# Optimization experiments

Measured on AMD Instinct MI355X. Metric: run time of the kernel, lower is better.

The kernel has to match this reference:

```python
import jax, jax.numpy as jnp
import numpy as np

B, T, C = 2, 2048, 2048
NH, NKV, D = 16, 4, 128
N_REP = NH // NKV
THETA = 10000.0


def setup_inputs() -> dict:
    key = jax.random.key(0)
    ks = jax.random.split(key, 5)
    s = 0.02
    return {
        "x": jax.random.normal(ks[0], (B, T, C), dtype=jnp.float32),
        "Wq": jax.random.normal(ks[1], (C, C), dtype=jnp.float32) * s,
        "Wk": jax.random.normal(ks[2], (NKV * D, C), dtype=jnp.float32) * s,
        "Wv": jax.random.normal(ks[3], (NKV * D, C), dtype=jnp.float32) * s,
        "Wo": jax.random.normal(ks[4], (C, C), dtype=jnp.float32) * s,
    }


def _rope(t):
    # t: (B, H, T, D); rotate pairs (even, odd) by angle pos * theta_i
    inv_freq = 1.0 / (THETA ** (jnp.arange(0, D, 2, dtype=jnp.float32) / D))  # (D/2,)
    ang = jnp.arange(T, dtype=jnp.float32)[:, None] * inv_freq[None, :]       # (T, D/2)
    cos, sin = jnp.cos(ang), jnp.sin(ang)
    te, to = t[..., 0::2], t[..., 1::2]
    re = te * cos - to * sin
    ro = te * sin + to * cos
    return jnp.stack([re, ro], axis=-1).reshape(t.shape).astype(t.dtype)


def reference(x, Wq, Wk, Wv, Wo):
    # Projections (Linear: y = x @ W.T)
    q = (x @ Wq.T).reshape(B, T, NH, D).transpose(0, 2, 1, 3)    # (B,NH,T,D)
    k = (x @ Wk.T).reshape(B, T, NKV, D).transpose(0, 2, 1, 3)   # (B,NKV,T,D)
    v = (x @ Wv.T).reshape(B, T, NKV, D).transpose(0, 2, 1, 3)
    q = _rope(q)
    k = _rope(k)
    # GQA: group query heads per kv head instead of materializing repeated K/V
    qg = q.reshape(B, NKV, N_REP, T, D)                          # (B,G,R,T,D)
    scale = 1.0 / jnp.sqrt(jnp.float32(D))
    scores = jnp.einsum("bgrtd,bgsd->bgrts", qg, k) * scale      # (B,G,R,T,T)
    causal = jnp.tril(jnp.ones((T, T), dtype=bool))
    scores = jnp.where(causal, scores, jnp.finfo(scores.dtype).min)
    attn = jax.nn.softmax(scores, axis=-1)
    out = jnp.einsum("bgrts,bgsd->bgrtd", attn, v)               # (B,G,R,T,D)
    out = out.reshape(B, NH, T, D).transpose(0, 2, 1, 3).reshape(B, T, C)
    return out @ Wo.T
```

## Files before the change

kernel.cpp:

```cpp
#include <hip/hip_runtime.h>
#include <hip/hip_bf16.h>
#include <stdint.h>

#define B_   2
#define T_   2048
#define C_   2048
#define NH_  16
#define NKV_ 4
#define D_   128
#define NREP_ 4

typedef __attribute__((ext_vector_type(8))) short bf16x8;
typedef __attribute__((ext_vector_type(4))) float f32x4;

__device__ inline short f2bs(float f) {
    __hip_bfloat16 h = __float2bfloat16(f);
    return *reinterpret_cast<short*>(&h);
}
__device__ inline float bs2f(unsigned short s) {
    __hip_bfloat16 h = *reinterpret_cast<__hip_bfloat16*>(&s);
    return __bfloat162float(h);
}

__device__ inline void gl_lds16(const __hip_bfloat16* g, __hip_bfloat16* l) {
    __builtin_amdgcn_global_load_lds(
        (const __attribute__((address_space(1))) unsigned int*)g,
        (__attribute__((address_space(3))) unsigned int*)l,
        16, 0, 0);
}

__global__ void cvt_f32_bf16(const float* __restrict__ src,
                             __hip_bfloat16* __restrict__ dst, int n) {
    int i = (blockIdx.x * blockDim.x + threadIdx.x) * 4;
    if (i >= n) return;
    float4 v = *reinterpret_cast<const float4*>(src + i);
    short4 o;
    o.x = f2bs(v.x); o.y = f2bs(v.y); o.z = f2bs(v.z); o.w = f2bs(v.w);
    *reinterpret_cast<short4*>(dst + i) = o;
}

__device__ inline void storeC(float* p, float v) { *p = v; }
__device__ inline void storeC(__hip_bfloat16* p, float v) { *p = __float2bfloat16(v); }

template <typename OutT>
__global__ __launch_bounds__(256) void gemm_bt(const __hip_bfloat16* __restrict__ A,
                                               const __hip_bfloat16* __restrict__ Bm,
                                               OutT* __restrict__ Cm,
                                               int M, int N, int K) {
    __shared__ __hip_bfloat16 As[128 * 32];
    __shared__ __hip_bfloat16 Bs[128 * 32];
    const int tid  = threadIdx.x;
    const int lane = tid & 63;
    const int wv   = tid >> 6;
    const int m0 = blockIdx.y * 128, n0 = blockIdx.x * 128;
    const int wm = (wv >> 1) * 64, wn = (wv & 1) * 64;
    const int q16 = lane >> 4, r16 = lane & 15;

    f32x4 acc[4][4] = {};

    const int lrow = tid >> 2;
    const int lcol = (tid & 3) * 8;
    const __hip_bfloat16* aG = A  + (size_t)(m0 + lrow) * K + lcol;
    const __hip_bfloat16* bG = Bm + (size_t)(n0 + lrow) * K + lcol;
    __hip_bfloat16* aL = As + tid * 8;
    __hip_bfloat16* bL = Bs + tid * 8;

    for (int k0 = 0; k0 < K; k0 += 32) {
        __syncthreads();
        gl_lds16(aG + k0,          aL);
        gl_lds16(aG + 64 * K + k0, aL + 2048);
        gl_lds16(bG + k0,          bL);
        gl_lds16(bG + 64 * K + k0, bL + 2048);
        __syncthreads();
        bf16x8 af[4], bfr[4];
#pragma unroll
        for (int i = 0; i < 4; i++)
            af[i] = *reinterpret_cast<const bf16x8*>(As + (wm + i * 16 + r16) * 32 + q16 * 8);
#pragma unroll
        for (int j = 0; j < 4; j++)
            bfr[j] = *reinterpret_cast<const bf16x8*>(Bs + (wn + j * 16 + r16) * 32 + q16 * 8);
#pragma unroll
        for (int i = 0; i < 4; i++)
#pragma unroll
            for (int j = 0; j < 4; j++)
                acc[i][j] = __builtin_amdgcn_mfma_f32_16x16x32_bf16(af[i], bfr[j], acc[i][j], 0, 0, 0);
    }

#pragma unroll
    for (int i = 0; i < 4; i++)
#pragma unroll
        for (int j = 0; j < 4; j++)
#pragma unroll
            for (int r = 0; r < 4; r++) {
                int row = m0 + wm + i * 16 + q16 * 4 + r;
                int col = n0 + wn + j * 16 + r16;
                storeC(&Cm[(size_t)row * N + col], acc[i][j][r]);
            }
}

__global__ void rope_scatter(const __hip_bfloat16* __restrict__ y,
                             __hip_bfloat16* __restrict__ qo,
                             __hip_bfloat16* __restrict__ ko,
                             __hip_bfloat16* __restrict__ vT) {
    int idx = blockIdx.x * blockDim.x + threadIdx.x;
    if (idx >= (B_ * T_) * 1536) return;
    int m = idx / 1536, pc = idx % 1536;
    int b = m / T_, t = m % T_;
    int n = pc * 2;
    ushort2 uv = *reinterpret_cast<const ushort2*>(y + (size_t)m * 3072 + n);
    float e = bs2f(uv.x), od = bs2f(uv.y);

    if (n < 2560) {
        int nn = (n < 2048) ? n : (n - 2048);
        int dloc = nn & 127;
        int p = dloc >> 1;
        float inv = __expf(-(float)p * (9.210340371976184f / 64.0f));
        float ang = (float)t * inv;
        float c = cosf(ang), s = sinf(ang);
        float re = e * c - od * s;
        float ro = e * s + od * c;
        ushort2 w;
        w.x = (unsigned short)f2bs(re);
        w.y = (unsigned short)f2bs(ro);
        if (n < 2048) {
            int h = n >> 7;
            *reinterpret_cast<ushort2*>(qo + ((size_t)(b * NH_ + h) * T_ + t) * D_ + dloc) = w;
        } else {
            int h = nn >> 7;
            *reinterpret_cast<ushort2*>(ko + ((size_t)(b * NKV_ + h) * T_ + t) * D_ + dloc) = w;
        }
    } else {
        int nn = n - 2560;
        int h = nn >> 7, d = nn & 127;
        __hip_bfloat16* base = vT + (size_t)(b * NKV_ + h) * D_ * T_;
        base[(size_t)d * T_ + t]       = __float2bfloat16(e);
        base[(size_t)(d + 1) * T_ + t] = __float2bfloat16(od);
    }
}

__global__ __launch_bounds__(256, 3) void attn_kernel(const __hip_bfloat16* __restrict__ Q,
                                                      const __hip_bfloat16* __restrict__ Kt,
                                                      const __hip_bfloat16* __restrict__ Vt,
                                                      __hip_bfloat16* __restrict__ Ao) {
    __shared__ __hip_bfloat16 Ks[2][4096];
    __shared__ __hip_bfloat16 Vs[2][4096];
    __shared__ __hip_bfloat16 Pl[4][1280];

    const int lane = threadIdx.x & 63, wv = threadIdx.x >> 6;
    const int bg = blockIdx.y;
    const int tb = (int)(gridDim.x - 1) - (int)blockIdx.x;
    const int b = bg >> 2, g = bg & 3;
    const int h = g * 4 + wv;
    const int t0 = tb * 32;
    const int q16 = lane >> 4, r16 = lane & 15;

    const __hip_bfloat16* qh = Q + ((size_t)((b * NH_ + h) * T_) + t0) * D_;
    const __hip_bfloat16* kh = Kt + (size_t)(b * NKV_ + g) * T_ * D_;
    const __hip_bfloat16* vh = Vt + (size_t)(b * NKV_ + g) * D_ * T_;

    bf16x8 bqA[4], bqB[4];
#pragma unroll
    for (int kk = 0; kk < 4; kk++) {
        bqA[kk] = *reinterpret_cast<const bf16x8*>(qh + (size_t)r16 * D_ + kk * 32 + q16 * 8);
        bqB[kk] = *reinterpret_cast<const bf16x8*>(qh + (size_t)(16 + r16) * D_ + kk * 32 + q16 * 8);
    }

    float liA = 0.f, liB = 0.f;
    f32x4 oA[8], oB[8];
#pragma unroll
    for (int d = 0; d < 8; d++) {
        oA[d] = (f32x4){0.f, 0.f, 0.f, 0.f};
        oB[d] = (f32x4){0.f, 0.f, 0.f, 0.f};
    }

    const float SCL2 = 0.088388347648318447f * 1.4426950408889634f;
    const int tqA = t0 + r16;
    const int tqB = t0 + 16 + r16;
    const int nIter = tb + 1;

    const __hip_bfloat16* gK = kh + (size_t)((wv & 1) * 16 + r16) * D_ + q16 * 8;
    const __hip_bfloat16* gV = vh + (size_t)(((wv - 2) * 4) * 16 + r16) * T_ + q16 * 8;

#define STAGE(bufi, s0_)                                                        \
    do {                                                                        \
        if (wv < 2) {                                                           \
            const __hip_bfloat16* gp = gK + (size_t)(s0_) * D_;                 \
            __hip_bfloat16* lp = &Ks[bufi][(wv * 4) * 512] + lane * 8;          \
            gl_lds16(gp,      lp);                                              \
            gl_lds16(gp + 32, lp + 512);                                        \
            gl_lds16(gp + 64, lp + 1024);                                       \
            gl_lds16(gp + 96, lp + 1536);                                       \
        } else {                                                                \
            const __hip_bfloat16* gp = gV + (s0_);                              \
            __hip_bfloat16* lp = &Vs[bufi][((wv - 2) * 4) * 512] + lane * 8;    \
            gl_lds16(gp,                      lp);                              \
            gl_lds16(gp + (size_t)16 * T_,    lp + 512);                        \
            gl_lds16(gp + (size_t)32 * T_,    lp + 1024);                       \
            gl_lds16(gp + (size_t)48 * T_,    lp + 1536);                       \
        }                                                                       \
    } while (0)

    STAGE(0, 0);

    for (int it = 0; it < nIter; it++) {
        const int s0 = it * 32;
        const int cur = it & 1;
        __syncthreads();
        if (it + 1 < nIter) STAGE(cur ^ 1, s0 + 32);

        f32x4 sc0A = (f32x4){0.f, 0.f, 0.f, 0.f};
        f32x4 sc1A = (f32x4){0.f, 0.f, 0.f, 0.f};
        f32x4 sc0B = (f32x4){0.f, 0.f, 0.f, 0.f};
        f32x4 sc1B = (f32x4){0.f, 0.f, 0.f, 0.f};
        {
            bf16x8 ak[4];
#pragma unroll
            for (int kk = 0; kk < 4; kk++)
                ak[kk] = *reinterpret_cast<const bf16x8*>(&Ks[cur][kk * 512] + lane * 8);
#pragma unroll
            for (int kk = 0; kk < 4; kk++) {
                sc0A = __builtin_amdgcn_mfma_f32_16x16x32_bf16(ak[kk], bqA[kk], sc0A, 0, 0, 0);
                sc0B = __builtin_amdgcn_mfma_f32_16x16x32_bf16(ak[kk], bqB[kk], sc0B, 0, 0, 0);
            }
#pragma unroll
            for (int kk = 0; kk < 4; kk++)
                ak[kk] = *reinterpret_cast<const bf16x8*>(&Ks[cur][(4 + kk) * 512] + lane * 8);
#pragma unroll
            for (int kk = 0; kk < 4; kk++) {
                sc1A = __builtin_amdgcn_mfma_f32_16x16x32_bf16(ak[kk], bqA[kk], sc1A, 0, 0, 0);
                sc1B = __builtin_amdgcn_mfma_f32_16x16x32_bf16(ak[kk], bqB[kk], sc1B, 0, 0, 0);
            }
        }

        ushort4 w0A, w1A, w0B, w1B;
        float psA = 0.f, psB = 0.f;
#pragma unroll
        for (int r = 0; r < 4; r++) {
            int s_a = s0 + q16 * 4 + r;
            float pa0 = (s_a <= tqA)      ? __builtin_amdgcn_exp2f(sc0A[r] * SCL2) : 0.f;
            float pa1 = (s_a + 16 <= tqA) ? __builtin_amdgcn_exp2f(sc1A[r] * SCL2) : 0.f;
            float pb0 = (s_a <= tqB)      ? __builtin_amdgcn_exp2f(sc0B[r] * SCL2) : 0.f;
            float pb1 = (s_a + 16 <= tqB) ? __builtin_amdgcn_exp2f(sc1B[r] * SCL2) : 0.f;
            psA += pa0 + pa1;
            psB += pb0 + pb1;
            ((unsigned short*)&w0A)[r] = (unsigned short)f2bs(pa0);
            ((unsigned short*)&w1A)[r] = (unsigned short)f2bs(pa1);
            ((unsigned short*)&w0B)[r] = (unsigned short)f2bs(pb0);
            ((unsigned short*)&w1B)[r] = (unsigned short)f2bs(pb1);
        }
        liA += psA;
        liB += psB;

        *reinterpret_cast<ushort4*>(&Pl[wv][r16 * 40 + q16 * 4]) = w0A;
        *reinterpret_cast<ushort4*>(&Pl[wv][r16 * 40 + 16 + q16 * 4]) = w1A;
        *reinterpret_cast<ushort4*>(&Pl[wv][640 + r16 * 40 + q16 * 4]) = w0B;
        *reinterpret_cast<ushort4*>(&Pl[wv][640 + r16 * 40 + 16 + q16 * 4]) = w1B;
        asm volatile("s_waitcnt lgkmcnt(0)" ::: "memory");
        bf16x8 pfA = *reinterpret_cast<const bf16x8*>(&Pl[wv][r16 * 40 + q16 * 8]);
        bf16x8 pfB = *reinterpret_cast<const bf16x8*>(&Pl[wv][640 + r16 * 40 + q16 * 8]);

#pragma unroll
        for (int d = 0; d < 8; d++) {
            bf16x8 bv = *reinterpret_cast<const bf16x8*>(&Vs[cur][d * 512] + lane * 8);
            oA[d] = __builtin_amdgcn_mfma_f32_16x16x32_bf16(pfA, bv, oA[d], 0, 0, 0);
            oB[d] = __builtin_amdgcn_mfma_f32_16x16x32_bf16(pfB, bv, oB[d], 0, 0, 0);
        }
    }

    liA += __shfl_xor(liA, 16);
    liA += __shfl_xor(liA, 32);
    liB += __shfl_xor(liB, 16);
    liB += __shfl_xor(liB, 32);
#pragma unroll
    for (int r = 0; r < 4; r++) {
        float lrA = __shfl(liA, q16 * 4 + r, 16);
        float lrB = __shfl(liB, q16 * 4 + r, 16);
        float invA = 1.0f / lrA;
        float invB = 1.0f / lrB;
        int tA = t0 + q16 * 4 + r;
        __hip_bfloat16* dstA = Ao + (size_t)(b * T_ + tA) * C_ + h * D_ + r16;
        __hip_bfloat16* dstB = dstA + (size_t)16 * C_;
#pragma unroll
        for (int d = 0; d < 8; d++) {
            dstA[d * 16] = __float2bfloat16(oA[d][r] * invA);
            dstB[d * 16] = __float2bfloat16(oB[d][r] * invB);
        }
    }
#undef STAGE
}

extern "C" void kernel_launch(void* const* d_in, const int* in_sizes, int n_in,
                              void* d_out, int out_size, void* d_ws, size_t ws_size,
                              hipStream_t stream) {
    const float* x  = (const float*)d_in[0];
    const float* Wq = (const float*)d_in[1];
    const float* Wk = (const float*)d_in[2];
    const float* Wv = (const float*)d_in[3];
    const float* Wo = (const float*)d_in[4];
    float* out = (float*)d_out;
    char* ws = (char*)d_ws;

    __hip_bfloat16* xb   = (__hip_bfloat16*)(ws + 0);
    __hip_bfloat16* wcat = (__hip_bfloat16*)(ws + 16777216);
    __hip_bfloat16* wob  = (__hip_bfloat16*)(ws + 29360128);
    __hip_bfloat16* yq   = (__hip_bfloat16*)(ws + 37748736);
    __hip_bfloat16* qatt = (__hip_bfloat16*)(ws + 62914560);
    __hip_bfloat16* katt = (__hip_bfloat16*)(ws + 79691776);
    __hip_bfloat16* vT   = (__hip_bfloat16*)(ws + 83886080);
    __hip_bfloat16* aout = (__hip_bfloat16*)(ws + 88080384);

    const int thr = 256;
    cvt_f32_bf16<<<(B_ * T_ * C_ / 4 + thr - 1) / thr, thr, 0, stream>>>(x, xb, B_ * T_ * C_);
    cvt_f32_bf16<<<(C_ * C_ / 4 + thr - 1) / thr, thr, 0, stream>>>(Wq, wcat, C_ * C_);
    cvt_f32_bf16<<<(512 * 2048 / 4 + thr - 1) / thr, thr, 0, stream>>>(Wk, wcat + C_ * C_, 512 * 2048);
    cvt_f32_bf16<<<(512 * 2048 / 4 + thr - 1) / thr, thr, 0, stream>>>(Wv, wcat + C_ * C_ + 512 * 2048, 512 * 2048);
    cvt_f32_bf16<<<(C_ * C_ / 4 + thr - 1) / thr, thr, 0, stream>>>(Wo, wob, C_ * C_);

    gemm_bt<__hip_bfloat16><<<dim3(24, 32), 256, 0, stream>>>(xb, wcat, yq, 4096, 3072, 2048);

    rope_scatter<<<(B_ * T_ * 1536 + thr - 1) / thr, thr, 0, stream>>>(yq, qatt, katt, vT);

    attn_kernel<<<dim3(64, 8), 256, 0, stream>>>(qatt, katt, vT, aout);

    gemm_bt<float><<<dim3(16, 32), 256, 0, stream>>>(aout, wob, out, 4096, 2048, 2048);
}
```

Before: 351.4 us.

## Split long causal attention rows into two KV halves with combine pass

Query tiles in the second half of the sequence are now handled by two blocks, each covering half of the KV range. Each writes unnormalized fp32 partial outputs and row sums to workspace, and a new combine kernel adds the halves and normalizes. This evens out the per-block work of causal attention and raises the block count from 512 to 768. Fully unmasked tiles also skip the causal compare. The split relies on the kernel having no running-max subtraction, so partial results add directly. The cost is extra fp32 traffic, one extra launch, and reuse of workspace regions (xb, yq) that are already dead at that point.

```diff
diff --git a/kernel.cpp b/kernel.cpp
--- a/kernel.cpp
+++ b/kernel.cpp
@@ -141,14 +141,23 @@
 __global__ __launch_bounds__(256, 3) void attn_kernel(const __hip_bfloat16* __restrict__ Q,
                                                       const __hip_bfloat16* __restrict__ Kt,
                                                       const __hip_bfloat16* __restrict__ Vt,
-                                                      __hip_bfloat16* __restrict__ Ao) {
+                                                      __hip_bfloat16* __restrict__ Ao,
+                                                      float* __restrict__ O0,
+                                                      float* __restrict__ O1,
+                                                      float* __restrict__ l0p,
+                                                      float* __restrict__ l1p) {
     __shared__ __hip_bfloat16 Ks[2][4096];
     __shared__ __hip_bfloat16 Vs[2][4096];
     __shared__ __hip_bfloat16 Pl[4][1280];
 
     const int lane = threadIdx.x & 63, wv = threadIdx.x >> 6;
     const int bg = blockIdx.y;
-    const int tb = (int)(gridDim.x - 1) - (int)blockIdx.x;
+    const int u  = (int)blockIdx.x;
+    int tb, nIt, sIdx;
+    if (u < 32)      { tb = u;      nIt = tb + 1;      sIdx = -1; }
+    else if (u < 64) { tb = u;      nIt = 32;          sIdx = 0;  }
+    else             { tb = u - 32; nIt = tb + 1 - 32; sIdx = 1;  }
+    const int sBase = (sIdx == 1) ? 1024 : 0;
     const int b = bg >> 2, g = bg & 3;
     const int h = g * 4 + wv;
     const int t0 = tb * 32;
@@ -176,7 +185,6 @@
     const float SCL2 = 0.088388347648318447f * 1.4426950408889634f;
     const int tqA = t0 + r16;
     const int tqB = t0 + 16 + r16;
-    const int nIter = tb + 1;
 
     const __hip_bfloat16* gK = kh + (size_t)((wv & 1) * 16 + r16) * D_ + q16 * 8;
     const __hip_bfloat16* gV = vh + (size_t)(((wv - 2) * 4) * 16 + r16) * T_ + q16 * 8;
@@ -200,13 +208,13 @@
         }                                                                       \
     } while (0)
 
-    STAGE(0, 0);
-
-    for (int it = 0; it < nIter; it++) {
-        const int s0 = it * 32;
-        const int cur = it & 1;
+    STAGE(0, sBase);
+
+    for (int j = 0; j < nIt; j++) {
+        const int s0 = sBase + j * 32;
+        const int cur = j & 1;
         __syncthreads();
-        if (it + 1 < nIter) STAGE(cur ^ 1, s0 + 32);
+        if (j + 1 < nIt) STAGE(cur ^ 1, s0 + 32);
 
         f32x4 sc0A = (f32x4){0.f, 0.f, 0.f, 0.f};
         f32x4 sc1A = (f32x4){0.f, 0.f, 0.f, 0.f};
@@ -234,19 +242,35 @@
 
         ushort4 w0A, w1A, w0B, w1B;
         float psA = 0.f, psB = 0.f;
-#pragma unroll
-        for (int r = 0; r < 4; r++) {
-            int s_a = s0 + q16 * 4 + r;
-            float pa0 = (s_a <= tqA)      ? __builtin_amdgcn_exp2f(sc0A[r] * SCL2) : 0.f;
-            float pa1 = (s_a + 16 <= tqA) ? __builtin_amdgcn_exp2f(sc1A[r] * SCL2) : 0.f;
-            float pb0 = (s_a <= tqB)      ? __builtin_amdgcn_exp2f(sc0B[r] * SCL2) : 0.f;
-            float pb1 = (s_a + 16 <= tqB) ? __builtin_amdgcn_exp2f(sc1B[r] * SCL2) : 0.f;
-            psA += pa0 + pa1;
-            psB += pb0 + pb1;
-            ((unsigned short*)&w0A)[r] = (unsigned short)f2bs(pa0);
-            ((unsigned short*)&w1A)[r] = (unsigned short)f2bs(pa1);
-            ((unsigned short*)&w0B)[r] = (unsigned short)f2bs(pb0);
-            ((unsigned short*)&w1B)[r] = (unsigned short)f2bs(pb1);
+        if (s0 + 32 > t0) {
+#pragma unroll
+            for (int r = 0; r < 4; r++) {
+                int s_a = s0 + q16 * 4 + r;
+                float pa0 = (s_a <= tqA)      ? __builtin_amdgcn_exp2f(sc0A[r] * SCL2) : 0.f;
+                float pa1 = (s_a + 16 <= tqA) ? __builtin_amdgcn_exp2f(sc1A[r] * SCL2) : 0.f;
+                float pb0 = (s_a <= tqB)      ? __builtin_amdgcn_exp2f(sc0B[r] * SCL2) : 0.f;
+                float pb1 = (s_a + 16 <= tqB) ? __builtin_amdgcn_exp2f(sc1B[r] * SCL2) : 0.f;
+                psA += pa0 + pa1;
+                psB += pb0 + pb1;
+                ((unsigned short*)&w0A)[r] = (unsigned short)f2bs(pa0);
+                ((unsigned short*)&w1A)[r] = (unsigned short)f2bs(pa1);
+                ((unsigned short*)&w0B)[r] = (unsigned short)f2bs(pb0);
+                ((unsigned short*)&w1B)[r] = (unsigned short)f2bs(pb1);
+            }
+        } else {
+#pragma unroll
+            for (int r = 0; r < 4; r++) {
+                float pa0 = __builtin_amdgcn_exp2f(sc0A[r] * SCL2);
+                float pa1 = __builtin_amdgcn_exp2f(sc1A[r] * SCL2);
+                float pb0 = __builtin_amdgcn_exp2f(sc0B[r] * SCL2);
+                float pb1 = __builtin_amdgcn_exp2f(sc1B[r] * SCL2);
+                psA += pa0 + pa1;
+                psB += pb0 + pb1;
+                ((unsigned short*)&w0A)[r] = (unsigned short)f2bs(pa0);
+                ((unsigned short*)&w1A)[r] = (unsigned short)f2bs(pa1);
+                ((unsigned short*)&w0B)[r] = (unsigned short)f2bs(pb0);
+                ((unsigned short*)&w1B)[r] = (unsigned short)f2bs(pb1);
+            }
         }
         liA += psA;
         liB += psB;
@@ -271,22 +295,62 @@
     liA += __shfl_xor(liA, 32);
     liB += __shfl_xor(liB, 16);
     liB += __shfl_xor(liB, 32);
-#pragma unroll
-    for (int r = 0; r < 4; r++) {
-        float lrA = __shfl(liA, q16 * 4 + r, 16);
-        float lrB = __shfl(liB, q16 * 4 + r, 16);
-        float invA = 1.0f / lrA;
-        float invB = 1.0f / lrB;
-        int tA = t0 + q16 * 4 + r;
-        __hip_bfloat16* dstA = Ao + (size_t)(b * T_ + tA) * C_ + h * D_ + r16;
-        __hip_bfloat16* dstB = dstA + (size_t)16 * C_;
-#pragma unroll
-        for (int d = 0; d < 8; d++) {
-            dstA[d * 16] = __float2bfloat16(oA[d][r] * invA);
-            dstB[d * 16] = __float2bfloat16(oB[d][r] * invB);
+
+    if (sIdx < 0) {
+#pragma unroll
+        for (int r = 0; r < 4; r++) {
+            float lrA = __shfl(liA, q16 * 4 + r, 16);
+            float lrB = __shfl(liB, q16 * 4 + r, 16);
+            float invA = 1.0f / lrA;
+            float invB = 1.0f / lrB;
+            int tA = t0 + q16 * 4 + r;
+            __hip_bfloat16* dstA = Ao + (size_t)(b * T_ + tA) * C_ + h * D_ + r16;
+            __hip_bfloat16* dstB = dstA + (size_t)16 * C_;
+#pragma unroll
+            for (int d = 0; d < 8; d++) {
+                dstA[d * 16] = __float2bfloat16(oA[d][r] * invA);
+                dstB[d * 16] = __float2bfloat16(oB[d][r] * invB);
+            }
+        }
+    } else {
+        float* Os = (sIdx == 0) ? O0 : O1;
+        float* ls = (sIdx == 0) ? l0p : l1p;
+        const size_t rb = (size_t)(b * NH_ + h) * 1024 + (size_t)(t0 - 1024);
+        if (q16 == 0) {
+            ls[rb + r16]      = liA;
+            ls[rb + 16 + r16] = liB;
+        }
+#pragma unroll
+        for (int r = 0; r < 4; r++) {
+            int rowl = q16 * 4 + r;
+            float* dA = Os + (rb + rowl) * 128 + r16;
+            float* dB = Os + (rb + 16 + rowl) * 128 + r16;
+#pragma unroll
+            for (int d = 0; d < 8; d++) {
+                dA[d * 16] = oA[d][r];
+                dB[d * 16] = oB[d][r];
+            }
         }
     }
 #undef STAGE
+}
+
+__global__ void attn_combine(const float* __restrict__ O0, const float* __restrict__ O1,
+                             const float* __restrict__ l0, const float* __restrict__ l1,
+                             __hip_bfloat16* __restrict__ Ao) {
+    int idx = blockIdx.x * blockDim.x + threadIdx.x;
+    int row = idx >> 5, d4 = (idx & 31) << 2;
+    int bh = row >> 10, tl = row & 1023;
+    int b = bh >> 4, h = bh & 15;
+    float inv = 1.0f / (l0[row] + l1[row]);
+    float4 a = *reinterpret_cast<const float4*>(O0 + (size_t)row * 128 + d4);
+    float4 c = *reinterpret_cast<const float4*>(O1 + (size_t)row * 128 + d4);
+    short4 o;
+    o.x = f2bs((a.x + c.x) * inv);
+    o.y = f2bs((a.y + c.y) * inv);
+    o.z = f2bs((a.z + c.z) * inv);
+    o.w = f2bs((a.w + c.w) * inv);
+    *reinterpret_cast<short4*>(Ao + (size_t)(b * T_ + 1024 + tl) * C_ + h * D_ + d4) = o;
 }
 
 extern "C" void kernel_launch(void* const* d_in, const int* in_sizes, int n_in,
@@ -309,6 +373,11 @@
     __hip_bfloat16* vT   = (__hip_bfloat16*)(ws + 83886080);
     __hip_bfloat16* aout = (__hip_bfloat16*)(ws + 88080384);
 
+    float* O0 = (float*)(ws + 0);
+    float* O1 = (float*)(ws + 37748736);
+    float* l0 = (float*)(ws + 37748736 + 16777216);
+    float* l1 = (float*)(ws + 37748736 + 16777216 + 131072);
+
     const int thr = 256;
     cvt_f32_bf16<<<(B_ * T_ * C_ / 4 + thr - 1) / thr, thr, 0, stream>>>(x, xb, B_ * T_ * C_);
     cvt_f32_bf16<<<(C_ * C_ / 4 + thr - 1) / thr, thr, 0, stream>>>(Wq, wcat, C_ * C_);
@@ -320,7 +389,8 @@
 
     rope_scatter<<<(B_ * T_ * 1536 + thr - 1) / thr, thr, 0, stream>>>(yq, qatt, katt, vT);
 
-    attn_kernel<<<dim3(64, 8), 256, 0, stream>>>(qatt, katt, vT, aout);
+    attn_kernel<<<dim3(96, 8), 256, 0, stream>>>(qatt, katt, vT, aout, O0, O1, l0, l1);
+    attn_combine<<<(2 * NH_ * 1024 * 32) / thr, thr, 0, stream>>>(O0, O1, l0, l1, aout);
 
     gemm_bt<float><<<dim3(16, 32), 256, 0, stream>>>(aout, wob, out, 4096, 2048, 2048);
 }
```

Result: faster. 330.6 us (-5.9%).
